# Kernel optimization log

Measured on AMD Instinct MI355X. Metric: run time of the kernel, lower is better.

## Reference

```python
import jax, jax.numpy as jnp
import numpy as np

N_NODES = 50000
N_EDGES = 400000
IN_F, HID_F, OUT_F = 768, 16, 21


def setup_inputs() -> dict:
    key = jax.random.key(0)
    ks = jax.random.split(key, 7)
    feature = jax.random.normal(ks[0], (N_NODES, IN_F), dtype=jnp.float32)
    W1 = jax.random.normal(ks[1], (IN_F, HID_F), dtype=jnp.float32) * 0.03
    b1 = jax.random.normal(ks[2], (HID_F,), dtype=jnp.float32) * 0.01
    W2 = jax.random.normal(ks[3], (HID_F, OUT_F), dtype=jnp.float32) * 0.1
    b2 = jax.random.normal(ks[4], (OUT_F,), dtype=jnp.float32) * 0.01
    src = jax.random.randint(ks[5], (N_EDGES,), 0, N_NODES, dtype=jnp.int32)
    dst = jax.random.randint(ks[6], (N_EDGES,), 0, N_NODES, dtype=jnp.int32)
    return {"feature": feature, "W1": W1, "b1": b1, "W2": W2, "b2": b2,
            "src": src, "dst": dst}


def _gcn_agg(h, src, dst):
    # copy_src + sum reduce: gather source features along edges, scatter-add to dst
    return jax.ops.segment_sum(h[src], dst, num_segments=N_NODES)


def reference(feature, W1, b1, W2, b2, src, dst):
    # layer 1: aggregate then linear + relu
    h = _gcn_agg(feature, src, dst)            # [N, 768]
    h = jax.nn.relu(h @ W1 + b1)               # [N, 16]
    # layer 2: aggregate then linear (no activation)
    h = _gcn_agg(h, src, dst)                  # [N, 16]
    return h @ W2 + b2                         # [N, 21]
```

## Files before the change

kernel.cpp:

```cpp
#include <hip/hip_runtime.h>

#define NN 50000
#define NE 400000
#define INF 768
#define HF 16
#define OF 21
#define ELLW 40

__global__ __launch_bounds__(256) void scatter_kernel(const int* __restrict__ src,
                                                      const int* __restrict__ dst,
                                                      int* __restrict__ cnt,
                                                      int* __restrict__ ell) {
    int e = blockIdx.x * 256 + threadIdx.x;
    if (e >= NE) return;
    int d = dst[e];
    int pos = atomicAdd(&cnt[d], 1);
    if (pos < ELLW) ell[d * ELLW + pos] = src[e];
}

#define FMA4(ACC, SS, VV) { (ACC).x += (SS)*(VV).x; (ACC).y += (SS)*(VV).y; \
                            (ACC).z += (SS)*(VV).z; (ACC).w += (SS)*(VV).w; }

__global__ __launch_bounds__(256) void gemm1_kernel(const float* __restrict__ F,
                                                    const float* __restrict__ W1,
                                                    float* __restrict__ P) {
    __shared__ float W1v[4 * INF * 4];

    const int t = threadIdx.x;
    for (int idx = t; idx < INF * HF; idx += 256) {
        int k = idx >> 4, j = idx & 15;
        W1v[(j >> 2) * (INF * 4) + k * 4 + (j & 3)] = W1[idx];
    }
    __syncthreads();

    int row = blockIdx.x * 64 + (t >> 2);
    const int q = t & 3;
    const bool active = row < NN;
    if (!active) row = NN - 1;

    const float* base = F + (size_t)row * INF + q * 4;
    float4 acc0 = {0,0,0,0}, acc1 = {0,0,0,0}, acc2 = {0,0,0,0}, acc3 = {0,0,0,0};

    float4 fa = *(const float4*)(base);
    float4 fb = *(const float4*)(base + 16);

#pragma unroll 4
    for (int i = 0; i < 48; ++i) {
        const int nx = i + 2;
        float4 fc = *(const float4*)(base + 16 * (nx < 48 ? nx : 0));
        const int kb = 16 * i + 4 * q;
#pragma unroll
        for (int m = 0; m < 4; ++m) {
            const float fm = (m == 0) ? fa.x : (m == 1) ? fa.y : (m == 2) ? fa.z : fa.w;
            const int ko = (kb + m) * 4;
            float4 w0 = *(const float4*)&W1v[0 * (INF * 4) + ko];
            float4 w1 = *(const float4*)&W1v[1 * (INF * 4) + ko];
            float4 w2 = *(const float4*)&W1v[2 * (INF * 4) + ko];
            float4 w3 = *(const float4*)&W1v[3 * (INF * 4) + ko];
            FMA4(acc0, fm, w0);
            FMA4(acc1, fm, w1);
            FMA4(acc2, fm, w2);
            FMA4(acc3, fm, w3);
        }
        fa = fb; fb = fc;
    }

#define BFLY(VAL) { VAL += __shfl_xor(VAL, 1); VAL += __shfl_xor(VAL, 2); }
    BFLY(acc0.x) BFLY(acc0.y) BFLY(acc0.z) BFLY(acc0.w)
    BFLY(acc1.x) BFLY(acc1.y) BFLY(acc1.z) BFLY(acc1.w)
    BFLY(acc2.x) BFLY(acc2.y) BFLY(acc2.z) BFLY(acc2.w)
    BFLY(acc3.x) BFLY(acc3.y) BFLY(acc3.z) BFLY(acc3.w)
#undef BFLY

    float4 ov;
    ov.x = (q == 0) ? acc0.x : (q == 1) ? acc1.x : (q == 2) ? acc2.x : acc3.x;
    ov.y = (q == 0) ? acc0.y : (q == 1) ? acc1.y : (q == 2) ? acc2.y : acc3.y;
    ov.z = (q == 0) ? acc0.z : (q == 1) ? acc1.z : (q == 2) ? acc2.z : acc3.z;
    ov.w = (q == 0) ? acc0.w : (q == 1) ? acc1.w : (q == 2) ? acc2.w : acc3.w;
    if (active)
        *(float4*)(P + (size_t)row * HF + q * 4) = ov;
}

__global__ __launch_bounds__(256) void agg1_kernel(const float* __restrict__ P,
                                                   const int* __restrict__ cnt,
                                                   const int* __restrict__ ell,
                                                   float* __restrict__ A1) {
    int g = blockIdx.x * 256 + threadIdx.x;
    int node = g >> 2;
    if (node >= NN) return;
    const int q = g & 3;
    int c = cnt[node]; if (c > ELLW) c = ELLW;
    const int* ep = ell + node * ELLW;
    float4 v = {0,0,0,0};
    for (int i = 0; i < c; ++i) {
        int s = ep[i];
        float4 p = *(const float4*)(P + (size_t)s * HF + q * 4);
        v.x += p.x; v.y += p.y; v.z += p.z; v.w += p.w;
    }
    *(float4*)(A1 + (size_t)node * HF + q * 4) = v;
}

__global__ __launch_bounds__(256) void agg2out_kernel(const float* __restrict__ A1,
                                                      const float* __restrict__ b1,
                                                      const int* __restrict__ cnt,
                                                      const int* __restrict__ ell,
                                                      const float* __restrict__ W2,
                                                      const float* __restrict__ b2,
                                                      float* __restrict__ out) {
    __shared__ float W2s[HF * OF];
    __shared__ float b2s[OF];
    const int t = threadIdx.x;
    for (int i = t; i < HF * OF; i += 256) W2s[i] = W2[i];
    if (t < OF) b2s[t] = b2[t];
    __syncthreads();

    int g = blockIdx.x * 256 + t;
    int node = g >> 2;
    if (node >= NN) return;
    const int q = g & 3;

    const float4 bb = *(const float4*)(b1 + q * 4);
    int c = cnt[node]; if (c > ELLW) c = ELLW;
    const int* ep = ell + node * ELLW;

    float4 v = {0,0,0,0};
    for (int i = 0; i < c; ++i) {
        int s = ep[i];
        float4 h = *(const float4*)(A1 + (size_t)s * HF + q * 4);
        h.x = fmaxf(h.x + bb.x, 0.0f);
        h.y = fmaxf(h.y + bb.y, 0.0f);
        h.z = fmaxf(h.z + bb.z, 0.0f);
        h.w = fmaxf(h.w + bb.w, 0.0f);
        v.x += h.x; v.y += h.y; v.z += h.z; v.w += h.w;
    }

    const float* w0 = W2s + (q * 4 + 0) * OF;
    const float* w1 = W2s + (q * 4 + 1) * OF;
    const float* w2 = W2s + (q * 4 + 2) * OF;
    const float* w3 = W2s + (q * 4 + 3) * OF;
    float o[OF];
#pragma unroll
    for (int cc = 0; cc < OF; ++cc)
        o[cc] = v.x * w0[cc] + v.y * w1[cc] + v.z * w2[cc] + v.w * w3[cc];
#pragma unroll
    for (int cc = 0; cc < OF; ++cc) {
        o[cc] += __shfl_xor(o[cc], 1);
        o[cc] += __shfl_xor(o[cc], 2);
    }
    float* op = out + (size_t)node * OF;
    for (int cc = q; cc < OF; cc += 4) op[cc] = o[cc] + b2s[cc];
}

extern "C" void kernel_launch(void* const* d_in, const int* in_sizes, int n_in,
                              void* d_out, int out_size, void* d_ws, size_t ws_size,
                              hipStream_t stream) {
    const float* F   = (const float*)d_in[0];
    const float* W1  = (const float*)d_in[1];
    const float* b1  = (const float*)d_in[2];
    const float* W2  = (const float*)d_in[3];
    const float* b2  = (const float*)d_in[4];
    const int*   src = (const int*)d_in[5];
    const int*   dst = (const int*)d_in[6];
    float* out = (float*)d_out;

    char* ws = (char*)d_ws;
    int*   cnt = (int*)(ws);
    int*   ell = (int*)(ws + 200192);
    float* P   = (float*)(ws + 8200192);
    float* A1  = (float*)(ws + 11400192);

    (void)hipMemsetAsync(cnt, 0, NN * sizeof(int), stream);
    scatter_kernel<<<(NE + 255) / 256, 256, 0, stream>>>(src, dst, cnt, ell);
    gemm1_kernel<<<(NN + 63) / 64, 256, 0, stream>>>(F, W1, P);
    agg1_kernel<<<(NN * 4 + 255) / 256, 256, 0, stream>>>(P, cnt, ell, A1);
    agg2out_kernel<<<(NN * 4 + 255) / 256, 256, 0, stream>>>(A1, b1, cnt, ell, W2, b2, out);
}
```

Baseline: 341.2 us.

## Use one thread per row in gemm1 and split edge loops across lanes

gemm1 now has each thread compute a full 16-wide output row. Blocks shrink to 64 threads, W1 is kept in natural row-major shared layout, and F is read through a 4-deep float4 register prefetch buffer, which removes the cross-lane butterfly reduction. Both aggregation kernels now use 16 lanes per node instead of 4, with each group of 4 lanes taking every fourth edge and combining through shuffles, to raise memory-level parallelism on the gathers. The risk is that per-thread row reads of F are strided by 3 KB between lanes, which makes loads uncoalesced. Small 64-thread blocks that each copy 48 KB of W1 may also cut occupancy and add redundant loads.

```diff
diff --git a/kernel.cpp b/kernel.cpp
--- a/kernel.cpp
+++ b/kernel.cpp
@@ -6,6 +6,9 @@
 #define HF 16
 #define OF 21
 #define ELLW 40
+
+#define FMA4(ACC, SS, VV) { (ACC).x += (SS)*(VV).x; (ACC).y += (SS)*(VV).y; \
+                            (ACC).z += (SS)*(VV).z; (ACC).w += (SS)*(VV).w; }
 
 __global__ __launch_bounds__(256) void scatter_kernel(const int* __restrict__ src,
                                                       const int* __restrict__ dst,
@@ -18,67 +21,50 @@
     if (pos < ELLW) ell[d * ELLW + pos] = src[e];
 }
 
-#define FMA4(ACC, SS, VV) { (ACC).x += (SS)*(VV).x; (ACC).y += (SS)*(VV).y; \
-                            (ACC).z += (SS)*(VV).z; (ACC).w += (SS)*(VV).w; }
+__global__ __launch_bounds__(64) void gemm1_kernel(const float* __restrict__ F,
+                                                   const float* __restrict__ W1,
+                                                   float* __restrict__ P) {
+    __shared__ float W1s[INF * HF];
 
-__global__ __launch_bounds__(256) void gemm1_kernel(const float* __restrict__ F,
-                                                    const float* __restrict__ W1,
-                                                    float* __restrict__ P) {
-    __shared__ float W1v[4 * INF * 4];
-
-    const int t = threadIdx.x;
-    for (int idx = t; idx < INF * HF; idx += 256) {
-        int k = idx >> 4, j = idx & 15;
-        W1v[(j >> 2) * (INF * 4) + k * 4 + (j & 3)] = W1[idx];
+    const int lane = threadIdx.x;
+    {
+        const float4* s = (const float4*)W1;
+        float4* d = (float4*)W1s;
+        for (int i = lane; i < (INF * HF) / 4; i += 64) d[i] = s[i];
     }
     __syncthreads();
 
-    int row = blockIdx.x * 64 + (t >> 2);
-    const int q = t & 3;
-    const bool active = row < NN;
-    if (!active) row = NN - 1;
+    int row = blockIdx.x * 64 + lane;
+    const bool act = row < NN;
+    if (!act) row = NN - 1;
+    const float4* fr = (const float4*)(F + (size_t)row * INF);
 
-    const float* base = F + (size_t)row * INF + q * 4;
     float4 acc0 = {0,0,0,0}, acc1 = {0,0,0,0}, acc2 = {0,0,0,0}, acc3 = {0,0,0,0};
-
-    float4 fa = *(const float4*)(base);
-    float4 fb = *(const float4*)(base + 16);
+    float4 buf[4];
+#pragma unroll
+    for (int i = 0; i < 4; ++i) buf[i] = fr[i];
 
 #pragma unroll 4
-    for (int i = 0; i < 48; ++i) {
-        const int nx = i + 2;
-        float4 fc = *(const float4*)(base + 16 * (nx < 48 ? nx : 0));
-        const int kb = 16 * i + 4 * q;
+    for (int c = 0; c < INF / 4; ++c) {
+        float4 fv = buf[c & 3];
+        if (c + 4 < INF / 4) buf[c & 3] = fr[c + 4];
+        const int kb = c * 4;
 #pragma unroll
         for (int m = 0; m < 4; ++m) {
-            const float fm = (m == 0) ? fa.x : (m == 1) ? fa.y : (m == 2) ? fa.z : fa.w;
-            const int ko = (kb + m) * 4;
-            float4 w0 = *(const float4*)&W1v[0 * (INF * 4) + ko];
-            float4 w1 = *(const float4*)&W1v[1 * (INF * 4) + ko];
-            float4 w2 = *(const float4*)&W1v[2 * (INF * 4) + ko];
-            float4 w3 = *(const float4*)&W1v[3 * (INF * 4) + ko];
+            const float fm = (m == 0) ? fv.x : (m == 1) ? fv.y : (m == 2) ? fv.z : fv.w;
+            const float4* wrow = (const float4*)&W1s[(kb + m) * HF];
+            float4 w0 = wrow[0], w1 = wrow[1], w2 = wrow[2], w3 = wrow[3];
             FMA4(acc0, fm, w0);
             FMA4(acc1, fm, w1);
             FMA4(acc2, fm, w2);
             FMA4(acc3, fm, w3);
         }
-        fa = fb; fb = fc;
     }
 
-#define BFLY(VAL) { VAL += __shfl_xor(VAL, 1); VAL += __shfl_xor(VAL, 2); }
-    BFLY(acc0.x) BFLY(acc0.y) BFLY(acc0.z) BFLY(acc0.w)
-    BFLY(acc1.x) BFLY(acc1.y) BFLY(acc1.z) BFLY(acc1.w)
-    BFLY(acc2.x) BFLY(acc2.y) BFLY(acc2.z) BFLY(acc2.w)
-    BFLY(acc3.x) BFLY(acc3.y) BFLY(acc3.z) BFLY(acc3.w)
-#undef BFLY
-
-    float4 ov;
-    ov.x = (q == 0) ? acc0.x : (q == 1) ? acc1.x : (q == 2) ? acc2.x : acc3.x;
-    ov.y = (q == 0) ? acc0.y : (q == 1) ? acc1.y : (q == 2) ? acc2.y : acc3.y;
-    ov.z = (q == 0) ? acc0.z : (q == 1) ? acc1.z : (q == 2) ? acc2.z : acc3.z;
-    ov.w = (q == 0) ? acc0.w : (q == 1) ? acc1.w : (q == 2) ? acc2.w : acc3.w;
-    if (active)
-        *(float4*)(P + (size_t)row * HF + q * 4) = ov;
+    if (act) {
+        float4* op = (float4*)(P + (size_t)row * HF);
+        op[0] = acc0; op[1] = acc1; op[2] = acc2; op[3] = acc3;
+    }
 }
 
 __global__ __launch_bounds__(256) void agg1_kernel(const float* __restrict__ P,
@@ -86,18 +72,23 @@
                                                    const int* __restrict__ ell,
                                                    float* __restrict__ A1) {
     int g = blockIdx.x * 256 + threadIdx.x;
-    int node = g >> 2;
+    int node = g >> 4;
     if (node >= NN) return;
-    const int q = g & 3;
+    const int l = g & 15, es = l >> 2, q = l & 3;
     int c = cnt[node]; if (c > ELLW) c = ELLW;
     const int* ep = ell + node * ELLW;
+
     float4 v = {0,0,0,0};
-    for (int i = 0; i < c; ++i) {
+    for (int i = es; i < c; i += 4) {
         int s = ep[i];
         float4 p = *(const float4*)(P + (size_t)s * HF + q * 4);
         v.x += p.x; v.y += p.y; v.z += p.z; v.w += p.w;
     }
-    *(float4*)(A1 + (size_t)node * HF + q * 4) = v;
+#define BFLY2(VAL) { VAL += __shfl_xor(VAL, 4); VAL += __shfl_xor(VAL, 8); }
+    BFLY2(v.x) BFLY2(v.y) BFLY2(v.z) BFLY2(v.w)
+#undef BFLY2
+    if (es == 0)
+        *(float4*)(A1 + (size_t)node * HF + q * 4) = v;
 }
 
 __global__ __launch_bounds__(256) void agg2out_kernel(const float* __restrict__ A1,
@@ -115,16 +106,16 @@
     __syncthreads();
 
     int g = blockIdx.x * 256 + t;
-    int node = g >> 2;
+    int node = g >> 4;
     if (node >= NN) return;
-    const int q = g & 3;
+    const int l = g & 15, es = l >> 2, q = l & 3;
 
     const float4 bb = *(const float4*)(b1 + q * 4);
     int c = cnt[node]; if (c > ELLW) c = ELLW;
     const int* ep = ell + node * ELLW;
 
     float4 v = {0,0,0,0};
-    for (int i = 0; i < c; ++i) {
+    for (int i = es; i < c; i += 4) {
         int s = ep[i];
         float4 h = *(const float4*)(A1 + (size_t)s * HF + q * 4);
         h.x = fmaxf(h.x + bb.x, 0.0f);
@@ -133,6 +124,9 @@
         h.w = fmaxf(h.w + bb.w, 0.0f);
         v.x += h.x; v.y += h.y; v.z += h.z; v.w += h.w;
     }
+#define BFLY2(VAL) { VAL += __shfl_xor(VAL, 4); VAL += __shfl_xor(VAL, 8); }
+    BFLY2(v.x) BFLY2(v.y) BFLY2(v.z) BFLY2(v.w)
+#undef BFLY2
 
     const float* w0 = W2s + (q * 4 + 0) * OF;
     const float* w1 = W2s + (q * 4 + 1) * OF;
@@ -147,8 +141,10 @@
         o[cc] += __shfl_xor(o[cc], 1);
         o[cc] += __shfl_xor(o[cc], 2);
     }
-    float* op = out + (size_t)node * OF;
-    for (int cc = q; cc < OF; cc += 4) op[cc] = o[cc] + b2s[cc];
+    if (es == 0) {
+        float* op = out + (size_t)node * OF;
+        for (int cc = q; cc < OF; cc += 4) op[cc] = o[cc] + b2s[cc];
+    }
 }
 
 extern "C" void kernel_launch(void* const* d_in, const int* in_sizes, int n_in,
@@ -171,7 +167,7 @@
 
     (void)hipMemsetAsync(cnt, 0, NN * sizeof(int), stream);
     scatter_kernel<<<(NE + 255) / 256, 256, 0, stream>>>(src, dst, cnt, ell);
-    gemm1_kernel<<<(NN + 63) / 64, 256, 0, stream>>>(F, W1, P);
-    agg1_kernel<<<(NN * 4 + 255) / 256, 256, 0, stream>>>(P, cnt, ell, A1);
-    agg2out_kernel<<<(NN * 4 + 255) / 256, 256, 0, stream>>>(A1, b1, cnt, ell, W2, b2, out);
+    gemm1_kernel<<<(NN + 63) / 64, 64, 0, stream>>>(F, W1, P);
+    agg1_kernel<<<(NN * 16 + 255) / 256, 256, 0, stream>>>(P, cnt, ell, A1);
+    agg2out_kernel<<<(NN * 16 + 255) / 256, 256, 0, stream>>>(A1, b1, cnt, ell, W2, b2, out);
 }
```

Result: slower. 355.4 us (+4.1%).
